# Kernel optimization log

Hardware: AMD Instinct MI355X
Metric: run time of the kernel (lower is better)

## Reference

```python
import jax, jax.numpy as jnp
import numpy as np

B, N, N_FEAT = 16, 1024, 128
N_LAYER, AGG_HIDDEN, FC_HIDDEN, N_CLASS = 3, 64, 128, 10
NEG_INF = -9e15
LEAKY_SLOPE = 0.2


def setup_inputs() -> dict:
    key = jax.random.key(0)
    ks = jax.random.split(key, 8)
    x = jax.random.normal(ks[0], (B, N, N_FEAT), dtype=jnp.float32)
    adj = jax.random.randint(ks[1], (B, N, N), 0, 2).astype(jnp.float32)
    # per-layer GAT params, stacked over layers
    Ws = jax.random.normal(ks[2], (N_LAYER, N_FEAT, AGG_HIDDEN), dtype=jnp.float32) * 0.1
    a1 = jax.random.normal(ks[3], (N_LAYER, AGG_HIDDEN), dtype=jnp.float32) * 0.1
    a2 = jax.random.normal(ks[4], (N_LAYER, AGG_HIDDEN), dtype=jnp.float32) * 0.1
    W1 = jax.random.normal(ks[5], (AGG_HIDDEN * N_LAYER, FC_HIDDEN), dtype=jnp.float32) * 0.05
    b1 = jnp.zeros((FC_HIDDEN,), dtype=jnp.float32)
    W2 = jax.random.normal(ks[6], (FC_HIDDEN, N_CLASS), dtype=jnp.float32) * 0.05
    b2 = jnp.zeros((N_CLASS,), dtype=jnp.float32)
    return {"x": x, "adj": adj, "Ws": Ws, "a1": a1, "a2": a2,
            "W1": W1, "b1": b1, "W2": W2, "b2": b2}


def _gat_layer(x, adj, W, a1, a2):
    # h: [B, N, H]
    h = jnp.einsum('bnf,fh->bnh', x, W)
    # e_ij = LeakyReLU(a1.h_i + a2.h_j)  -- split-a trick, avoids [B,N,N,2H]
    f1 = jnp.einsum('bnh,h->bn', h, a1)
    f2 = jnp.einsum('bnh,h->bn', h, a2)
    e = jax.nn.leaky_relu(f1[:, :, None] + f2[:, None, :], LEAKY_SLOPE)  # [B,N,N]
    att = jax.nn.softmax(jnp.where(adj > 0, e, NEG_INF), axis=-1)
    return jnp.einsum('bnm,bmh->bnh', att, h)


def reference(x, adj, Ws, a1, a2, W1, b1, W2, b2):
    # eval mode: dropout is identity
    outs = [jax.nn.relu(_gat_layer(x, adj, Ws[i], a1[i], a2[i]))
            for i in range(N_LAYER)]
    h = jnp.concatenate(outs, axis=2)          # [B, N, H*L]
    pooled = jnp.mean(h, axis=1)               # 'avg' pool over nodes -> [B, H*L]
    z = jax.nn.relu(pooled @ W1 + b1)
    return jax.nn.softmax(z @ W2 + b2, axis=-1)  # [B, n_class]
```

## Files before the change

### kernel.cpp

```cpp
#include <hip/hip_runtime.h>

#define B 16
#define N 1024
#define NF 128
#define NL 3
#define AH 64
#define HC 192
#define FCH 128
#define NC 10
#define L2E 1.44269504088896f

typedef __attribute__((ext_vector_type(8))) short bf16x8;
typedef __attribute__((ext_vector_type(4))) float f32x4;
typedef __attribute__((ext_vector_type(4))) unsigned int u32x4;

static __device__ __forceinline__ unsigned short f2bf(float f) {
  unsigned int x = __builtin_bit_cast(unsigned int, f);
  return (unsigned short)((x + 0x7fffu + ((x >> 16) & 1u)) >> 16);
}
static __device__ __forceinline__ float bf2f(unsigned short u) {
  unsigned int x = ((unsigned int)u) << 16;
  return __builtin_bit_cast(float, x);
}

__global__ __launch_bounds__(256, 2) void k_feat(
    const float* __restrict__ x, const float* __restrict__ Ws,
    const float* __restrict__ a1, const float* __restrict__ a2,
    unsigned short* __restrict__ h_f, float* __restrict__ f1g,
    float* __restrict__ f2g, float* __restrict__ pooled)
{
  __shared__ float xs[64][132];
  __shared__ unsigned short wl[2][64][136];
  unsigned short (*hlds)[72] = (unsigned short(*)[72])&xs[0][0];
  const int t = threadIdx.x;
  const int n0g = blockIdx.x * 64;
  const int gb = n0g >> 10, nl0 = n0g & 1023;
  const int wv = t >> 6, lane = t & 63;
  const int lr = lane & 15, lg = lane >> 4;
  const int lrow = wv * 16 + lr;
  const int wcol = t & 63, woct = t >> 6;

  if (blockIdx.x == 0) {
    #pragma unroll
    for (int i = 0; i < 12; ++i) pooled[i * 256 + t] = 0.f;
  }

#define LOADW(R, L) {                                                         \
    _Pragma("unroll")                                                         \
    for (int p = 0; p < 4; ++p) {                                             \
      const int oct = p * 4 + woct;                                           \
      _Pragma("unroll")                                                       \
      for (int i = 0; i < 8; ++i)                                             \
        R[p][i] = Ws[((size_t)(L) * NF + oct * 8 + i) * AH + wcol];           \
    } }
#define WRITEW(R) {                                                           \
    _Pragma("unroll")                                                         \
    for (int p = 0; p < 4; ++p) {                                             \
      const int oct = p * 4 + woct;                                           \
      bf16x8 hv, lv;                                                          \
      _Pragma("unroll")                                                       \
      for (int i = 0; i < 8; ++i) {                                           \
        const unsigned short hi = f2bf(R[p][i]);                              \
        hv[i] = (short)hi;                                                    \
        lv[i] = (short)f2bf(R[p][i] - bf2f(hi));                              \
      }                                                                       \
      *(bf16x8*)&wl[0][wcol][oct * 8] = hv;                                   \
      *(bf16x8*)&wl[1][wcol][oct * 8] = lv;                                   \
    } }
#define MFMAL(L) {                                                            \
    _Pragma("unroll")                                                         \
    for (int n2 = 0; n2 < 4; ++n2) {                                          \
      const int n = (L) * 4 + n2;                                             \
      _Pragma("unroll")                                                       \
      for (int kf = 0; kf < 4; ++kf) {                                        \
        const bf16x8 whi = *(const bf16x8*)&wl[0][n2 * 16 + lr][kf * 32 + lg * 8]; \
        const bf16x8 wlo = *(const bf16x8*)&wl[1][n2 * 16 + lr][kf * 32 + lg * 8]; \
        acc[n] = __builtin_amdgcn_mfma_f32_16x16x32_bf16(xhi[kf], whi, acc[n], 0, 0, 0); \
        acc[n] = __builtin_amdgcn_mfma_f32_16x16x32_bf16(xhi[kf], wlo, acc[n], 0, 0, 0); \
        acc[n] = __builtin_amdgcn_mfma_f32_16x16x32_bf16(xlo[kf], whi, acc[n], 0, 0, 0); \
      }                                                                       \
    } }

  float wrA[4][8], wrB[4][8];
  LOADW(wrA, 0);

  #pragma unroll
  for (int p = 0; p < 8; ++p) {
    const int q = p * 256 + t;
    const int row = q >> 5, c4 = (q & 31) * 4;
    *(float4*)&xs[row][c4] = *(const float4*)&x[(size_t)(n0g + row) * NF + c4];
  }
  __syncthreads();

  bf16x8 xhi[4], xlo[4];
  #pragma unroll
  for (int kf = 0; kf < 4; ++kf) {
    const float4 q0 = *(const float4*)&xs[lrow][kf * 32 + lg * 8];
    const float4 q1 = *(const float4*)&xs[lrow][kf * 32 + lg * 8 + 4];
    const float xv[8] = {q0.x, q0.y, q0.z, q0.w, q1.x, q1.y, q1.z, q1.w};
    #pragma unroll
    for (int e = 0; e < 8; ++e) {
      const unsigned short hi = f2bf(xv[e]);
      xhi[kf][e] = (short)hi;
      xlo[kf][e] = (short)f2bf(xv[e] - bf2f(hi));
    }
  }

  f32x4 acc[12];
  #pragma unroll
  for (int n = 0; n < 12; ++n) acc[n] = (f32x4){0.f, 0.f, 0.f, 0.f};

  WRITEW(wrA);
  LOADW(wrB, 1);
  __syncthreads();
  MFMAL(0);
  __syncthreads();
  WRITEW(wrB);
  LOADW(wrA, 2);
  __syncthreads();
  MFMAL(1);
  __syncthreads();
  WRITEW(wrA);
  __syncthreads();
  MFMAL(2);

#undef LOADW
#undef WRITEW
#undef MFMAL

  float s1[3][4], s2[3][4];
  #pragma unroll
  for (int l = 0; l < 3; ++l)
    #pragma unroll
    for (int r = 0; r < 4; ++r) { s1[l][r] = 0.f; s2[l][r] = 0.f; }
  #pragma unroll
  for (int n = 0; n < 12; ++n) {
    const int col = n * 16 + lr;
    const float a1v = a1[col] * L2E, a2v = a2[col] * L2E;
    const int l = n >> 2;
    #pragma unroll
    for (int r = 0; r < 4; ++r) {
      s1[l][r] += acc[n][r] * a1v;
      s2[l][r] += acc[n][r] * a2v;
    }
  }
  #pragma unroll
  for (int off = 1; off < 16; off <<= 1)
    #pragma unroll
    for (int l = 0; l < 3; ++l)
      #pragma unroll
      for (int r = 0; r < 4; ++r) {
        s1[l][r] += __shfl_xor(s1[l][r], off);
        s2[l][r] += __shfl_xor(s2[l][r], off);
      }
  if (lr == 0) {
    #pragma unroll
    for (int l = 0; l < 3; ++l)
      #pragma unroll
      for (int r = 0; r < 4; ++r) {
        const int rw = n0g + wv * 16 + lg * 4 + r;
        f1g[(size_t)l * (B * N) + rw] = s1[l][r];
        f2g[(size_t)l * (B * N) + rw] = s2[l][r];
      }
  }

  __syncthreads();
  #pragma unroll
  for (int n = 0; n < 12; ++n) {
    const int col = n * 16 + lr;
    #pragma unroll
    for (int rp = 0; rp < 2; ++rp) {
      const unsigned int pr = (unsigned int)f2bf(acc[n][rp * 2]) |
                              ((unsigned int)f2bf(acc[n][rp * 2 + 1]) << 16);
      *(unsigned int*)&hlds[col][wv * 16 + lg * 4 + rp * 2] = pr;
    }
  }
  __syncthreads();
  #pragma unroll
  for (int p = 0; p < 6; ++p) {
    const int widx = p * 256 + t;
    const int lane_w = widx & 63;
    const int jb2 = (widx >> 6) & 1;
    const int n_w = (widx >> 7) & 3;
    const int l_w = widx >> 9;
    const int col = l_w * 64 + n_w * 16 + (lane_w & 15);
    const int jloc = jb2 * 32 + (lane_w >> 4) * 8;
    const size_t off =
        ((((size_t)(gb * 3 + l_w) * 4 + n_w) * 32 + (nl0 >> 5) + jb2) * 64 + lane_w) * 8;
    *(uint4*)&h_f[off] = *(const uint4*)&hlds[col][jloc];
  }
}

__global__ __launch_bounds__(256) void k_tab(
    const float* __restrict__ f1, const float* __restrict__ f2,
    unsigned int* __restrict__ tabuv, float* __restrict__ tabA,
    float* __restrict__ tabC)
{
  __shared__ float red[4];
  const int lb = blockIdx.x, t = threadIdx.x;
  const float* f2p = f2 + (size_t)lb * N;
  const float* f1p = f1 + (size_t)lb * N;

  float v = -1e30f;
  #pragma unroll
  for (int i = 0; i < 4; ++i) v = fmaxf(v, f2p[i * 256 + t]);
  #pragma unroll
  for (int off = 32; off; off >>= 1) v = fmaxf(v, __shfl_down(v, off));
  if ((t & 63) == 0) red[t >> 6] = v;
  __syncthreads();
  const float mx = fmaxf(fmaxf(red[0], red[1]), fmaxf(red[2], red[3]));

  #pragma unroll
  for (int i = 0; i < 4; ++i) {
    const int j = i * 256 + t;
    const float q2 = f2p[j];
    const float q1 = f1p[j];
    const float tt = q1 + mx;
    const float sr = fmaxf(tt, 0.f) + 0.2f * fminf(tt, 0.f);
    tabuv[(size_t)lb * N + j] =
        (unsigned int)f2bf(exp2f(q2)) | ((unsigned int)f2bf(exp2f(0.2f * q2)) << 16);
    tabA[(size_t)lb * N + j] = exp2f(q1 - sr);
    tabC[(size_t)lb * N + j] = exp2f(0.2f * q1 - sr);
  }
}

__global__ __launch_bounds__(64) void k_att(
    const float* __restrict__ adj, const unsigned short* __restrict__ h_f,
    const unsigned int* __restrict__ tabuv, const float* __restrict__ tabA,
    const float* __restrict__ tabC, float* __restrict__ pooled)
{
  const int bid = blockIdx.x;
  const int idx = (bid & 7) * 384 + (bid >> 3);
  const int stripe = idx / 3;
  const int l = idx - stripe * 3;
  const int b = stripe >> 6;
  const int i0 = (stripe & 63) * 16;
  const int lane = threadIdx.x;
  const int lr = lane & 15, lg = lane >> 4;
  const int msh = (lg & 1) * 8;

  __shared__ unsigned short sm[16][66];
  __shared__ unsigned int uvp[N];

  const float* ap = adj + ((size_t)(b * N + i0)) * N;
  #pragma unroll 4
  for (int i = 0; i < 16; ++i) {
    const float* p = ap + (size_t)i * N + lane * 16;
    unsigned int bits = 0;
    #pragma unroll
    for (int qq = 0; qq < 4; ++qq) {
      const uint4 u = *(const uint4*)(p + qq * 4);
      bits |= (u.x ? 1u : 0u) << (qq * 4 + 0);
      bits |= (u.y ? 1u : 0u) << (qq * 4 + 1);
      bits |= (u.z ? 1u : 0u) << (qq * 4 + 2);
      bits |= (u.w ? 1u : 0u) << (qq * 4 + 3);
    }
    sm[i][lane] = (unsigned short)bits;
  }

  const int lb = l * B + b;
  #pragma unroll
  for (int i = 0; i < 4; ++i)
    *(uint4*)&uvp[i * 256 + lane * 4] =
        *(const uint4*)&tabuv[(size_t)lb * N + i * 256 + lane * 4];

  const float A = tabA[(size_t)lb * N + i0 + lr];
  const float C = tabC[(size_t)lb * N + i0 + lr];

  const unsigned short* hfb = h_f + ((size_t)(b * 3 + l)) * 65536;
  const bf16x8 ones = {(short)0x3F80, (short)0x3F80, (short)0x3F80, (short)0x3F80,
                       (short)0x3F80, (short)0x3F80, (short)0x3F80, (short)0x3F80};

  f32x4 acc[4];
  #pragma unroll
  for (int n = 0; n < 4; ++n) acc[n] = (f32x4){0.f, 0.f, 0.f, 0.f};
  f32x4 accd = (f32x4){0.f, 0.f, 0.f, 0.f};

  __syncthreads();

#define LOADJ(BUF, MW, J) {                                                   \
    const int jj = (J) & (N - 1);                                             \
    const int jt = jj >> 6;                                                   \
    const unsigned int s0 = sm[lr][jt * 4 + (lg >> 1)];                       \
    const unsigned int s1 = sm[lr][jt * 4 + 2 + (lg >> 1)];                   \
    MW = ((s0 >> msh) & 0xffu) | (((s1 >> msh) & 0xffu) << 8);                \
    _Pragma("unroll")                                                         \
    for (int q = 0; q < 8; ++q) {                                             \
      const int ks = q >> 2, n = q & 3;                                       \
      BUF[q] = *(const bf16x8*)&hfb[(((size_t)n * 32 + (jj >> 5) + ks) * 64 + \
                                     lane) * 8];                              \
    } }

#define COMPJ(BUF, MW, J) {                                                   \
    _Pragma("unroll")                                                         \
    for (int ks = 0; ks < 2; ++ks) {                                          \
      const int kb = ((J) & (N - 1)) + ks * 32 + lg * 8;                      \
      const uint4 w0 = *(const uint4*)&uvp[kb];                               \
      const uint4 w1 = *(const uint4*)&uvp[kb + 4];                           \
      const unsigned int wk[8] = {w0.x, w0.y, w0.z, w0.w,                     \
                                  w1.x, w1.y, w1.z, w1.w};                    \
      const unsigned int mby = ((MW) >> (ks * 8)) & 0xffu;                    \
      unsigned int pk[4];                                                     \
      _Pragma("unroll")                                                       \
      for (int ep = 0; ep < 4; ++ep) {                                        \
        unsigned int pr[2];                                                   \
        _Pragma("unroll")                                                     \
        for (int h = 0; h < 2; ++h) {                                         \
          const int e = ep * 2 + h;                                           \
          const float ue = __builtin_bit_cast(float, wk[e] << 16);            \
          const float ve = __builtin_bit_cast(float, wk[e] & 0xffff0000u);    \
                  \
          const float p = fmaxf(A * ue, C * ve);                              \
          const unsigned int sel =                                            \
              (unsigned int)(((int)(mby << (31 - e))) >> 31);                 \
          pr[h] = (__builtin_bit_cast(unsigned int, p) + 0x8000u) & sel;      \
        }                                                                     \
        pk[ep] = __builtin_amdgcn_perm(pr[1], pr[0], 0x07060302u);            \
      }                                                                       \
      const u32x4 pkv = {pk[0], pk[1], pk[2], pk[3]};                         \
      const bf16x8 av = __builtin_bit_cast(bf16x8, pkv);                      \
      _Pragma("unroll")                                                       \
      for (int n = 0; n < 4; ++n)                                             \
        acc[n] = __builtin_amdgcn_mfma_f32_16x16x32_bf16(av, BUF[ks * 4 + n], \
                                                         acc[n], 0, 0, 0);    \
      accd = __builtin_amdgcn_mfma_f32_16x16x32_bf16(av, ones, accd, 0, 0, 0);\
    } }

#define SBAR __builtin_amdgcn_sched_barrier(0)

  bf16x8 bA[8], bB[8];
  unsigned int mwA, mwB;
  LOADJ(bA, mwA, 0);
  SBAR;
  for (int j0 = 0; j0 < N; j0 += 128) {
    LOADJ(bB, mwB, j0 + 64);
    SBAR;
    COMPJ(bA, mwA, j0);
    SBAR;
    LOADJ(bA, mwA, j0 + 128);
    SBAR;
    COMPJ(bB, mwB, j0 + 64);
    SBAR;
  }
#undef LOADJ
#undef COMPJ
#undef SBAR

  float dn[4];
  #pragma unroll
  for (int r = 0; r < 4; ++r) dn[r] = 1.f / fmaxf(accd[r], 1e-37f);

  #pragma unroll
  for (int n = 0; n < 4; ++n) {
    float csum = 0.f;
    #pragma unroll
    for (int r = 0; r < 4; ++r) csum += fmaxf(acc[n][r] * dn[r], 0.f);
    csum += __shfl_xor(csum, 16);
    csum += __shfl_xor(csum, 32);
    if (lg == 0) atomicAdd(&pooled[b * HC + l * 64 + n * 16 + lr], csum);
  }
}

__global__ __launch_bounds__(192) void k_head(
    const float* __restrict__ pooled_sums, const float* __restrict__ W1,
    const float* __restrict__ b1, const float* __restrict__ W2,
    const float* __restrict__ b2, float* __restrict__ out)
{
  const int b = blockIdx.x, t = threadIdx.x;
  __shared__ float pooled[HC];
  __shared__ float z[FCH];
  __shared__ float logits[NC];

  if (t < HC) pooled[t] = pooled_sums[b * HC + t] * (1.f / (float)N);
  __syncthreads();

  if (t < FCH) {
    float a = b1[t];
    #pragma unroll 4
    for (int f = 0; f < HC; ++f) a += pooled[f] * W1[(size_t)f * FCH + t];
    z[t] = a > 0.f ? a : 0.f;
  }
  __syncthreads();

  if (t < NC) {
    float a = b2[t];
    #pragma unroll 4
    for (int f = 0; f < FCH; ++f) a += z[f] * W2[(size_t)f * NC + t];
    logits[t] = a;
  }
  __syncthreads();

  if (t == 0) {
    float mxl = logits[0];
    for (int c = 1; c < NC; ++c) mxl = fmaxf(mxl, logits[c]);
    float e[NC], sum = 0.f;
    for (int c = 0; c < NC; ++c) { e[c] = __expf(logits[c] - mxl); sum += e[c]; }
    const float inv = 1.f / sum;
    for (int c = 0; c < NC; ++c) out[b * NC + c] = e[c] * inv;
  }
}

extern "C" void kernel_launch(void* const* d_in, const int* in_sizes, int n_in,
                              void* d_out, int out_size, void* d_ws, size_t ws_size,
                              hipStream_t stream)
{
  const float* x   = (const float*)d_in[0];
  const float* adj = (const float*)d_in[1];
  const float* Ws  = (const float*)d_in[2];
  const float* a1  = (const float*)d_in[3];
  const float* a2  = (const float*)d_in[4];
  const float* W1  = (const float*)d_in[5];
  const float* b1  = (const float*)d_in[6];
  const float* W2  = (const float*)d_in[7];
  const float* b2  = (const float*)d_in[8];
  float* out = (float*)d_out;

  unsigned short* h_f   = (unsigned short*)d_ws;
  float*          f1    = (float*)(h_f + (size_t)B * HC * N);
  float*          f2    = f1 + (size_t)NL * B * N;
  float*          pooled= f2 + (size_t)NL * B * N;
  unsigned int*   tabuv = (unsigned int*)(pooled + B * HC + 16);
  float*          tabA  = (float*)(tabuv + (size_t)NL * B * N);
  float*          tabC  = tabA + (size_t)NL * B * N;

  k_feat<<<256, 256, 0, stream>>>(x, Ws, a1, a2, h_f, f1, f2, pooled);
  k_tab <<<NL * B, 256, 0, stream>>>(f1, f2, tabuv, tabA, tabC);
  k_att <<<3072, 64, 0, stream>>>(adj, h_f, tabuv, tabA, tabC, pooled);
  k_head<<<B, 192, 0, stream>>>(pooled, W1, b1, W2, b2, out);
}
```

Baseline: 74.89 us.

## Split attention key range across two waves per block with LDS reduction

Result: no change. 75.98 us (+1.5%).

```diff
diff --git a/kernel.cpp b/kernel.cpp
--- a/kernel.cpp
+++ b/kernel.cpp
@@ -224,7 +224,7 @@
   }
 }
 
-__global__ __launch_bounds__(64) void k_att(
+__global__ __launch_bounds__(128) void k_att(
     const float* __restrict__ adj, const unsigned short* __restrict__ h_f,
     const unsigned int* __restrict__ tabuv, const float* __restrict__ tabA,
     const float* __restrict__ tabC, float* __restrict__ pooled)
@@ -235,17 +235,21 @@
   const int l = idx - stripe * 3;
   const int b = stripe >> 6;
   const int i0 = (stripe & 63) * 16;
-  const int lane = threadIdx.x;
+  const int t = threadIdx.x;
+  const int w = t >> 6, lane = t & 63;
   const int lr = lane & 15, lg = lane >> 4;
   const int msh = (lg & 1) * 8;
+  const int base = w * 512;
 
   __shared__ unsigned short sm[16][66];
   __shared__ unsigned int uvp[N];
+  __shared__ float cmb[64][21];
 
   const float* ap = adj + ((size_t)(b * N + i0)) * N;
-  #pragma unroll 4
-  for (int i = 0; i < 16; ++i) {
-    const float* p = ap + (size_t)i * N + lane * 16;
+  #pragma unroll
+  for (int i = 0; i < 8; ++i) {
+    const int row = w * 8 + i;
+    const float* p = ap + (size_t)row * N + lane * 16;
     unsigned int bits = 0;
     #pragma unroll
     for (int qq = 0; qq < 4; ++qq) {
@@ -255,14 +259,15 @@
       bits |= (u.z ? 1u : 0u) << (qq * 4 + 2);
       bits |= (u.w ? 1u : 0u) << (qq * 4 + 3);
     }
-    sm[i][lane] = (unsigned short)bits;
+    sm[row][lane] = (unsigned short)bits;
   }
 
   const int lb = l * B + b;
   #pragma unroll
-  for (int i = 0; i < 4; ++i)
-    *(uint4*)&uvp[i * 256 + lane * 4] =
-        *(const uint4*)&tabuv[(size_t)lb * N + i * 256 + lane * 4];
+  for (int i = 0; i < 2; ++i) {
+    const int o = (w * 2 + i) * 256 + lane * 4;
+    *(uint4*)&uvp[o] = *(const uint4*)&tabuv[(size_t)lb * N + o];
+  }
 
   const float A = tabA[(size_t)lb * N + i0 + lr];
   const float C = tabC[(size_t)lb * N + i0 + lr];
@@ -279,7 +284,7 @@
   __syncthreads();
 
 #define LOADJ(BUF, MW, J) {                                                   \
-    const int jj = (J) & (N - 1);                                             \
+    const int jj = base | ((J) & 511);                                        \
     const int jt = jj >> 6;                                                   \
     const unsigned int s0 = sm[lr][jt * 4 + (lg >> 1)];                       \
     const unsigned int s1 = sm[lr][jt * 4 + 2 + (lg >> 1)];                   \
@@ -292,9 +297,10 @@
     } }
 
 #define COMPJ(BUF, MW, J) {                                                   \
+    const int jjc = base | ((J) & 511);                                       \
     _Pragma("unroll")                                                         \
     for (int ks = 0; ks < 2; ++ks) {                                          \
-      const int kb = ((J) & (N - 1)) + ks * 32 + lg * 8;                      \
+      const int kb = jjc + ks * 32 + lg * 8;                                  \
       const uint4 w0 = *(const uint4*)&uvp[kb];                               \
       const uint4 w1 = *(const uint4*)&uvp[kb + 4];                           \
       const unsigned int wk[8] = {w0.x, w0.y, w0.z, w0.w,                     \
@@ -332,7 +338,7 @@
   unsigned int mwA, mwB;
   LOADJ(bA, mwA, 0);
   SBAR;
-  for (int j0 = 0; j0 < N; j0 += 128) {
+  for (int j0 = 0; j0 < 512; j0 += 128) {
     LOADJ(bB, mwB, j0 + 64);
     SBAR;
     COMPJ(bA, mwA, j0);
@@ -346,18 +352,36 @@
 #undef COMPJ
 #undef SBAR
 
-  float dn[4];
-  #pragma unroll
-  for (int r = 0; r < 4; ++r) dn[r] = 1.f / fmaxf(accd[r], 1e-37f);
-
-  #pragma unroll
-  for (int n = 0; n < 4; ++n) {
-    float csum = 0.f;
-    #pragma unroll
-    for (int r = 0; r < 4; ++r) csum += fmaxf(acc[n][r] * dn[r], 0.f);
-    csum += __shfl_xor(csum, 16);
-    csum += __shfl_xor(csum, 32);
-    if (lg == 0) atomicAdd(&pooled[b * HC + l * 64 + n * 16 + lr], csum);
+  if (w == 1) {
+    #pragma unroll
+    for (int n = 0; n < 4; ++n)
+      #pragma unroll
+      for (int r = 0; r < 4; ++r) cmb[lane][n * 4 + r] = acc[n][r];
+    #pragma unroll
+    for (int r = 0; r < 4; ++r) cmb[lane][16 + r] = accd[r];
+  }
+  __syncthreads();
+  if (w == 0) {
+    #pragma unroll
+    for (int n = 0; n < 4; ++n)
+      #pragma unroll
+      for (int r = 0; r < 4; ++r) acc[n][r] += cmb[lane][n * 4 + r];
+    #pragma unroll
+    for (int r = 0; r < 4; ++r) accd[r] += cmb[lane][16 + r];
+
+    float dn[4];
+    #pragma unroll
+    for (int r = 0; r < 4; ++r) dn[r] = 1.f / fmaxf(accd[r], 1e-37f);
+
+    #pragma unroll
+    for (int n = 0; n < 4; ++n) {
+      float csum = 0.f;
+      #pragma unroll
+      for (int r = 0; r < 4; ++r) csum += fmaxf(acc[n][r] * dn[r], 0.f);
+      csum += __shfl_xor(csum, 16);
+      csum += __shfl_xor(csum, 32);
+      if (lg == 0) atomicAdd(&pooled[b * HC + l * 64 + n * 16 + lr], csum);
+    }
   }
 }
 
@@ -425,6 +449,6 @@
 
   k_feat<<<256, 256, 0, stream>>>(x, Ws, a1, a2, h_f, f1, f2, pooled);
   k_tab <<<NL * B, 256, 0, stream>>>(f1, f2, tabuv, tabA, tabC);
-  k_att <<<3072, 64, 0, stream>>>(adj, h_f, tabuv, tabA, tabC, pooled);
+  k_att <<<3072, 128, 0, stream>>>(adj, h_f, tabuv, tabA, tabC, pooled);
   k_head<<<B, 192, 0, stream>>>(pooled, W1, b1, W2, b2, out);
 }
```

## Share adjacency mask across layers and stage h tiles via direct-to-LDS loads

Applied to the files above, without the earlier changes.

After: 91.28 us. +21.9%, slower.

```diff
diff --git a/kernel.cpp b/kernel.cpp
--- a/kernel.cpp
+++ b/kernel.cpp
@@ -21,6 +21,13 @@
 static __device__ __forceinline__ float bf2f(unsigned short u) {
   unsigned int x = ((unsigned int)u) << 16;
   return __builtin_bit_cast(float, x);
+}
+
+static __device__ __forceinline__ void gload_lds16(const unsigned short* g,
+                                                   unsigned short* s) {
+  __builtin_amdgcn_global_load_lds(
+      (const __attribute__((address_space(1))) void*)g,
+      (__attribute__((address_space(3))) void*)s, 16, 0, 0);
 }
 
 __global__ __launch_bounds__(256, 2) void k_feat(
@@ -224,28 +231,30 @@
   }
 }
 
-__global__ __launch_bounds__(64) void k_att(
+__global__ __launch_bounds__(384) void k_att(
     const float* __restrict__ adj, const unsigned short* __restrict__ h_f,
     const unsigned int* __restrict__ tabuv, const float* __restrict__ tabA,
     const float* __restrict__ tabC, float* __restrict__ pooled)
 {
   const int bid = blockIdx.x;
-  const int idx = (bid & 7) * 384 + (bid >> 3);
-  const int stripe = idx / 3;
-  const int l = idx - stripe * 3;
-  const int b = stripe >> 6;
-  const int i0 = (stripe & 63) * 16;
-  const int lane = threadIdx.x;
+  const int blk = (bid & 7) * 64 + (bid >> 3);
+  const int b = blk >> 5;
+  const int i0 = (blk & 31) * 32;
+  const int t = threadIdx.x;
+  const int w = t >> 6, lane = t & 63;
+  const int l = w >> 1, g = w & 1;
   const int lr = lane & 15, lg = lane >> 4;
   const int msh = (lg & 1) * 8;
-
-  __shared__ unsigned short sm[16][66];
-  __shared__ unsigned int uvp[N];
+  const int jrow = g * 16 + lr;
+
+  __shared__ unsigned short sm[32][66];
+  __shared__ unsigned int uvp[NL][N];
+  __shared__ unsigned short stage[NL][2][8][512];
 
   const float* ap = adj + ((size_t)(b * N + i0)) * N;
-  #pragma unroll 4
-  for (int i = 0; i < 16; ++i) {
-    const float* p = ap + (size_t)i * N + lane * 16;
+  for (int q = t; q < 2048; q += 384) {
+    const int row = q >> 6, ch = q & 63;
+    const float* p = ap + (size_t)row * N + ch * 16;
     unsigned int bits = 0;
     #pragma unroll
     for (int qq = 0; qq < 4; ++qq) {
@@ -255,19 +264,20 @@
       bits |= (u.z ? 1u : 0u) << (qq * 4 + 2);
       bits |= (u.w ? 1u : 0u) << (qq * 4 + 3);
     }
-    sm[i][lane] = (unsigned short)bits;
+    sm[row][ch] = (unsigned short)bits;
+  }
+
+  for (int q = t; q < 768; q += 384) {
+    const int ll = q >> 8, o4 = (q & 255) * 4;
+    *(uint4*)&uvp[ll][o4] = *(const uint4*)&tabuv[(size_t)(ll * B + b) * N + o4];
   }
 
   const int lb = l * B + b;
-  #pragma unroll
-  for (int i = 0; i < 4; ++i)
-    *(uint4*)&uvp[i * 256 + lane * 4] =
-        *(const uint4*)&tabuv[(size_t)lb * N + i * 256 + lane * 4];
-
-  const float A = tabA[(size_t)lb * N + i0 + lr];
-  const float C = tabC[(size_t)lb * N + i0 + lr];
+  const float A = tabA[(size_t)lb * N + i0 + jrow];
+  const float C = tabC[(size_t)lb * N + i0 + jrow];
 
   const unsigned short* hfb = h_f + ((size_t)(b * 3 + l)) * 65536;
+  const unsigned int* uvl = &uvp[l][0];
   const bf16x8 ones = {(short)0x3F80, (short)0x3F80, (short)0x3F80, (short)0x3F80,
                        (short)0x3F80, (short)0x3F80, (short)0x3F80, (short)0x3F80};
 
@@ -276,30 +286,31 @@
   for (int n = 0; n < 4; ++n) acc[n] = (f32x4){0.f, 0.f, 0.f, 0.f};
   f32x4 accd = (f32x4){0.f, 0.f, 0.f, 0.f};
 
-  __syncthreads();
-
-#define LOADJ(BUF, MW, J) {                                                   \
-    const int jj = (J) & (N - 1);                                             \
-    const int jt = jj >> 6;                                                   \
-    const unsigned int s0 = sm[lr][jt * 4 + (lg >> 1)];                       \
-    const unsigned int s1 = sm[lr][jt * 4 + 2 + (lg >> 1)];                   \
-    MW = ((s0 >> msh) & 0xffu) | (((s1 >> msh) & 0xffu) << 8);                \
-    _Pragma("unroll")                                                         \
-    for (int q = 0; q < 8; ++q) {                                             \
-      const int ks = q >> 2, n = q & 3;                                       \
-      BUF[q] = *(const bf16x8*)&hfb[(((size_t)n * 32 + (jj >> 5) + ks) * 64 + \
-                                     lane) * 8];                              \
+#define ISSUE(BUF, JT) {                                                      \
+    _Pragma("unroll")                                                         \
+    for (int i = 0; i < 4; ++i) {                                             \
+      const int q = g * 4 + i;                                                \
+      const int n_ = q & 3, ks_ = q >> 2;                                     \
+      gload_lds16(hfb + ((size_t)(n_ * 32 + 2 * (JT) + ks_)) * 512 + lane * 8,\
+                  &stage[l][BUF][q][0]);                                      \
     } }
 
-#define COMPJ(BUF, MW, J) {                                                   \
+#define COMPJ(BUF, JT) {                                                      \
+    bf16x8 bfr[8];                                                            \
+    _Pragma("unroll")                                                         \
+    for (int q = 0; q < 8; ++q)                                               \
+      bfr[q] = *(const bf16x8*)&stage[l][BUF][q][lane * 8];                   \
+    const unsigned int s0_ = sm[jrow][(JT) * 4 + (lg >> 1)];                  \
+    const unsigned int s1_ = sm[jrow][(JT) * 4 + 2 + (lg >> 1)];              \
+    const unsigned int MW = ((s0_ >> msh) & 0xffu) | (((s1_ >> msh) & 0xffu) << 8); \
     _Pragma("unroll")                                                         \
     for (int ks = 0; ks < 2; ++ks) {                                          \
-      const int kb = ((J) & (N - 1)) + ks * 32 + lg * 8;                      \
-      const uint4 w0 = *(const uint4*)&uvp[kb];                               \
-      const uint4 w1 = *(const uint4*)&uvp[kb + 4];                           \
+      const int kb = (JT) * 64 + ks * 32 + lg * 8;                            \
+      const uint4 w0 = *(const uint4*)&uvl[kb];                               \
+      const uint4 w1 = *(const uint4*)&uvl[kb + 4];                           \
       const unsigned int wk[8] = {w0.x, w0.y, w0.z, w0.w,                     \
                                   w1.x, w1.y, w1.z, w1.w};                    \
-      const unsigned int mby = ((MW) >> (ks * 8)) & 0xffu;                    \
+      const unsigned int mby = (MW >> (ks * 8)) & 0xffu;                      \
       unsigned int pk[4];                                                     \
       _Pragma("unroll")                                                       \
       for (int ep = 0; ep < 4; ++ep) {                                        \
@@ -321,30 +332,24 @@
       const bf16x8 av = __builtin_bit_cast(bf16x8, pkv);                      \
       _Pragma("unroll")                                                       \
       for (int n = 0; n < 4; ++n)                                             \
-        acc[n] = __builtin_amdgcn_mfma_f32_16x16x32_bf16(av, BUF[ks * 4 + n], \
+        acc[n] = __builtin_amdgcn_mfma_f32_16x16x32_bf16(av, bfr[ks * 4 + n], \
                                                          acc[n], 0, 0, 0);    \
       accd = __builtin_amdgcn_mfma_f32_16x16x32_bf16(av, ones, accd, 0, 0, 0);\
     } }
 
-#define SBAR __builtin_amdgcn_sched_barrier(0)
-
-  bf16x8 bA[8], bB[8];
-  unsigned int mwA, mwB;
-  LOADJ(bA, mwA, 0);
-  SBAR;
-  for (int j0 = 0; j0 < N; j0 += 128) {
-    LOADJ(bB, mwB, j0 + 64);
-    SBAR;
-    COMPJ(bA, mwA, j0);
-    SBAR;
-    LOADJ(bA, mwA, j0 + 128);
-    SBAR;
-    COMPJ(bB, mwB, j0 + 64);
-    SBAR;
-  }
-#undef LOADJ
+  int buf = 0;
+  ISSUE(0, 0);
+  for (int jt = 0; jt < 16; ++jt) {
+    ISSUE(buf ^ 1, jt + 1);
+    asm volatile("s_waitcnt vmcnt(4)" ::: "memory");
+    __builtin_amdgcn_sched_barrier(0);
+    __syncthreads();
+    COMPJ(buf, jt);
+    __syncthreads();
+    buf ^= 1;
+  }
+#undef ISSUE
 #undef COMPJ
-#undef SBAR
 
   float dn[4];
   #pragma unroll
@@ -425,6 +430,6 @@
 
   k_feat<<<256, 256, 0, stream>>>(x, Ws, a1, a2, h_f, f1, f2, pooled);
   k_tab <<<NL * B, 256, 0, stream>>>(f1, f2, tabuv, tabA, tabC);
-  k_att <<<3072, 64, 0, stream>>>(adj, h_f, tabuv, tabA, tabC, pooled);
+  k_att <<<512, 384, 0, stream>>>(adj, h_f, tabuv, tabA, tabC, pooled);
   k_head<<<B, 192, 0, stream>>>(pooled, W1, b1, W2, b2, out);
 }
```
